# Kernel optimization log

Measured on AMD Instinct MI355X. Metric: run time of the kernel, lower is better.

The kernel has to match this reference:

```python
import math
import jax, jax.numpy as jnp
import numpy as np

EMBED = 512
HEADS = 8
EPS = 1e-5


def _ln(x, gamma, beta):
    mu = jnp.mean(x, axis=-1, keepdims=True)
    var = jnp.mean(jnp.square(x - mu), axis=-1, keepdims=True)
    return (x - mu) * jax.lax.rsqrt(var + EPS) * gamma + beta


def setup_inputs() -> dict:
    key = jax.random.key(0)
    ks = jax.random.split(key, 16)
    D = EMBED
    s = 0.02
    inp = {
        "moves_embeddings": jax.random.normal(ks[0], (4, 2048, D), dtype=jnp.float32),
        "wq": jax.random.normal(ks[1], (D, D), dtype=jnp.float32) * s,
        "bq": jnp.zeros((D,), jnp.float32),
        "wk": jax.random.normal(ks[2], (D, D), dtype=jnp.float32) * s,
        "bk": jnp.zeros((D,), jnp.float32),
        "wv": jax.random.normal(ks[3], (D, D), dtype=jnp.float32) * s,
        "bv": jnp.zeros((D,), jnp.float32),
        "wo": jax.random.normal(ks[4], (D, D), dtype=jnp.float32) * s,
        "bo": jnp.zeros((D,), jnp.float32),
        "w_up": jax.random.normal(ks[5], (D, 4 * D), dtype=jnp.float32) * s,
        "b_up": jnp.zeros((4 * D,), jnp.float32),
        "w_down": jax.random.normal(ks[6], (4 * D, D), dtype=jnp.float32) * s,
        "b_down": jnp.zeros((D,), jnp.float32),
        "g1": jnp.ones((D,), jnp.float32),
        "beta1": jnp.zeros((D,), jnp.float32),
        "g2": jnp.ones((D,), jnp.float32),
        "beta2": jnp.zeros((D,), jnp.float32),
    }
    return inp


def reference(moves_embeddings, wq, bq, wk, bk, wv, bv, wo, bo,
              w_up, b_up, w_down, b_down, g1, beta1, g2, beta2):
    x = moves_embeddings  # [B, S, D]
    B, S, D = x.shape
    Hd = D // HEADS
    # QKV projections, split heads -> [B, H, S, Hd]
    q = (x @ wq + bq).reshape(B, S, HEADS, Hd).transpose(0, 2, 1, 3)
    k = (x @ wk + bk).reshape(B, S, HEADS, Hd).transpose(0, 2, 1, 3)
    v = (x @ wv + bv).reshape(B, S, HEADS, Hd).transpose(0, 2, 1, 3)
    # NOTE: original scales by sqrt(embedding_dim), not sqrt(head_dim)
    scores = jnp.einsum('bhqd,bhkd->bhqk', q, k) / math.sqrt(D)
    attn = jax.nn.softmax(scores, axis=-1)
    ctx = jnp.einsum('bhqk,bhkd->bhqd', attn, v)
    ctx = ctx.transpose(0, 2, 1, 3).reshape(B, S, D)
    y = ctx @ wo + bo
    x = _ln(x + y, g1, beta1)
    # FFN with exact (erf) GELU, matching torch nn.GELU default
    h = jax.nn.gelu(x @ w_up + b_up, approximate=False)
    y = h @ w_down + b_down
    return _ln(x + y, g2, beta2)
```

## Files before the change

kernel.cpp:

```cpp
#include <hip/hip_runtime.h>
#include <math.h>

#define D 512
#define NHEADS 8
#define HD 64
#define SEQ 2048
#define BATCH 4
#define MROWS (BATCH*SEQ)
#define QKVSTR 1536
#define ATT_QSCALE 0.06376228841159383f

typedef short bf16x8 __attribute__((ext_vector_type(8)));
typedef float f32x4 __attribute__((ext_vector_type(4)));
typedef float f32x16 __attribute__((ext_vector_type(16)));

__device__ __forceinline__ ushort f2bf(float f) {
    union { float f; unsigned u; } v; v.f = f;
    unsigned r = (v.u + 0x7fffu + ((v.u >> 16) & 1u)) >> 16;
    return (ushort)r;
}
__device__ __forceinline__ float bf2f(ushort u) {
    union { unsigned u; float f; } v; v.u = ((unsigned)u) << 16; return v.f;
}

__device__ __forceinline__ unsigned cvt_pk_bf16(float lo, float hi_) {
    unsigned r;
    asm("v_cvt_pk_bf16_f32 %0, %1, %2" : "=v"(r) : "v"(lo), "v"(hi_));
    return r;
}

__device__ __forceinline__ float exp2_hw(float x) {
    float r;
    asm("v_exp_f32 %0, %1" : "=v"(r) : "v"(x));
    return r;
}

__device__ __forceinline__ void plswap(unsigned &a, unsigned &b) {
    asm("v_permlane32_swap_b32 %0, %1" : "+v"(a), "+v"(b));
}
__device__ __forceinline__ void plswapf(float &a, float &b) {
    union { float f; unsigned u; } ua, ub;
    ua.f = a; ub.f = b;
    asm("v_permlane32_swap_b32 %0, %1" : "+v"(ua.u), "+v"(ub.u));
    a = ua.f; b = ub.f;
}

__device__ __forceinline__ void gload16(const void* g, void* lds) {
    __builtin_amdgcn_global_load_lds(
        (const __attribute__((address_space(1))) unsigned int*)(uintptr_t)g,
        (__attribute__((address_space(3))) unsigned int*)(uintptr_t)lds,
        16, 0, 0);
}

__device__ __forceinline__ int xcd_swz(int wg, int nwg) {
    const int cpx = nwg >> 3;
    return (wg & 7) * cpx + (wg >> 3);
}

template<int GELU, int OBF16, int SPLITK>
__global__ __launch_bounds__(512)
void gemm_mfma8(const ushort* __restrict__ A, const ushort* __restrict__ Bt,
                const float* __restrict__ bias, void* __restrict__ Cp,
                void* __restrict__ Cp2, int M, int N, int K)
{
    __shared__ ushort As[2][128 * 64];
    __shared__ ushort Bs[2][128 * 64];

    const int tid = threadIdx.x;
    const int w = tid >> 6, lane = tid & 63;
    const int lr = lane & 15, lg = lane >> 4;
    const int wr = w >> 2, wc = w & 3;

    const int gx = gridDim.x;
    const int wg = xcd_swz(blockIdx.y * gx + blockIdx.x, gx * gridDim.y);
    const int row0 = (wg / gx) * 128, col0 = (wg % gx) * 128;

    const int kLen = SPLITK ? (K >> 1) : K;
    const int kOff = SPLITK ? blockIdx.z * kLen : 0;

    const int srow = lane >> 3;
    const int schunk = (lane & 7) ^ srow;

    const ushort* aSrc = A  + (size_t)(row0 + w * 16 + srow) * K + kOff + schunk * 8;
    const ushort* bSrc = Bt + (size_t)(col0 + w * 16 + srow) * K + kOff + schunk * 8;

    f32x4 acc[4][2] = {};

    auto STAGE = [&](int buf, int k0) {
        ushort* aD = &As[buf][(w * 16) * 64];
        ushort* bD = &Bs[buf][(w * 16) * 64];
        gload16(aSrc + k0,                 aD);
        gload16(aSrc + (size_t)8 * K + k0, aD + 8 * 64);
        gload16(bSrc + k0,                 bD);
        gload16(bSrc + (size_t)8 * K + k0, bD + 8 * 64);
    };

    auto COMPUTE = [&](int buf) {
        const ushort* AsB = As[buf];
        const ushort* BsB = Bs[buf];
        #pragma unroll
        for (int kc = 0; kc < 2; ++kc) {
            bf16x8 af[4], bfr[2];
            #pragma unroll
            for (int mt = 0; mt < 4; ++mt)
                af[mt] = *(const bf16x8*)&AsB[(wr * 64 + mt * 16 + lr) * 64 +
                                             (((kc * 4 + lg) ^ (lr & 7)) * 8)];
            #pragma unroll
            for (int nt = 0; nt < 2; ++nt)
                bfr[nt] = *(const bf16x8*)&BsB[(wc * 32 + nt * 16 + lr) * 64 +
                                              (((kc * 4 + lg) ^ (lr & 7)) * 8)];
            __builtin_amdgcn_s_setprio(1);
            #pragma unroll
            for (int mt = 0; mt < 4; ++mt)
                #pragma unroll
                for (int nt = 0; nt < 2; ++nt)
                    acc[mt][nt] = __builtin_amdgcn_mfma_f32_16x16x32_bf16(
                        af[mt], bfr[nt], acc[mt][nt], 0, 0, 0);
            __builtin_amdgcn_s_setprio(0);
        }
    };

    const int nk = kLen >> 6;
    STAGE(0, 0);
    __syncthreads();
    for (int t = 0; t < nk; ++t) {
        if (t + 1 < nk) STAGE((t + 1) & 1, (t + 1) << 6);
        COMPUTE(t & 1);
        __syncthreads();
    }

    float* Pp = SPLITK ? (blockIdx.z ? (float*)Cp2 : (float*)Cp) : (float*)Cp;
    #pragma unroll
    for (int nt = 0; nt < 2; ++nt) {
        const int col = col0 + wc * 32 + nt * 16 + lr;
        const float bv = SPLITK ? 0.f : bias[col];
        #pragma unroll
        for (int mt = 0; mt < 4; ++mt) {
            #pragma unroll
            for (int i = 0; i < 4; ++i) {
                float o = acc[mt][nt][i] + bv;
                if (GELU) o = 0.5f * o * (1.0f + erff(o * 0.70710678118654752f));
                const size_t idx = (size_t)(row0 + wr * 64 + mt * 16 + lg * 4 + i) * N + col;
                if (OBF16) ((ushort*)Cp)[idx] = f2bf(o);
                else       Pp[idx] = o;
            }
        }
    }
}

__global__ __launch_bounds__(512)
void gemm_qkv8(const ushort* __restrict__ A, const ushort* __restrict__ Bt,
               const float* __restrict__ bias, ushort* __restrict__ qkv,
               ushort* __restrict__ vt)
{
    __shared__ ushort As[2][128 * 64];
    __shared__ ushort Bs[2][128 * 64];

    const int tid = threadIdx.x;
    const int w = tid >> 6, lane = tid & 63;
    const int lr = lane & 15, lg = lane >> 4;
    const int wr = w >> 2, wc = w & 3;

    const int gx = gridDim.x;
    const int wg = xcd_swz(blockIdx.y * gx + blockIdx.x, gx * gridDim.y);
    const int row0 = (wg / gx) * 128, col0 = (wg % gx) * 128;

    const int K = 512;

    const int srow = lane >> 3;
    const int schunk = (lane & 7) ^ srow;

    const ushort* aSrc = A  + (size_t)(row0 + w * 16 + srow) * K + schunk * 8;
    const ushort* bSrc = Bt + (size_t)(col0 + w * 16 + srow) * K + schunk * 8;

    f32x4 acc[4][2] = {};

    auto STAGE = [&](int buf, int k0) {
        ushort* aD = &As[buf][(w * 16) * 64];
        ushort* bD = &Bs[buf][(w * 16) * 64];
        gload16(aSrc + k0,                 aD);
        gload16(aSrc + (size_t)8 * K + k0, aD + 8 * 64);
        gload16(bSrc + k0,                 bD);
        gload16(bSrc + (size_t)8 * K + k0, bD + 8 * 64);
    };

    auto COMPUTE = [&](int buf) {
        const ushort* AsB = As[buf];
        const ushort* BsB = Bs[buf];
        #pragma unroll
        for (int kc = 0; kc < 2; ++kc) {
            bf16x8 af[4], bfr[2];
            #pragma unroll
            for (int mt = 0; mt < 4; ++mt)
                af[mt] = *(const bf16x8*)&AsB[(wr * 64 + mt * 16 + lr) * 64 +
                                             (((kc * 4 + lg) ^ (lr & 7)) * 8)];
            #pragma unroll
            for (int nt = 0; nt < 2; ++nt)
                bfr[nt] = *(const bf16x8*)&BsB[(wc * 32 + nt * 16 + lr) * 64 +
                                              (((kc * 4 + lg) ^ (lr & 7)) * 8)];
            __builtin_amdgcn_s_setprio(1);
            #pragma unroll
            for (int mt = 0; mt < 4; ++mt)
                #pragma unroll
                for (int nt = 0; nt < 2; ++nt)
                    acc[mt][nt] = __builtin_amdgcn_mfma_f32_16x16x32_bf16(
                        af[mt], bfr[nt], acc[mt][nt], 0, 0, 0);
            __builtin_amdgcn_s_setprio(0);
        }
    };

    STAGE(0, 0);
    __syncthreads();
    for (int t = 0; t < 8; ++t) {
        if (t + 1 < 8) STAGE((t + 1) & 1, (t + 1) << 6);
        COMPUTE(t & 1);
        __syncthreads();
    }

    #pragma unroll
    for (int nt = 0; nt < 2; ++nt) {
        const int col = col0 + wc * 32 + nt * 16 + lr;
        const float bv = bias[col];
        if (col < 1024) {
            const float sc = (col < 512) ? ATT_QSCALE : 1.0f;
            #pragma unroll
            for (int mt = 0; mt < 4; ++mt) {
                #pragma unroll
                for (int i = 0; i < 4; ++i) {
                    const float o = (acc[mt][nt][i] + bv) * sc;
                    qkv[(size_t)(row0 + wr * 64 + mt * 16 + lg * 4 + i) * QKVSTR + col] = f2bf(o);
                }
            }
        } else {
            const int hh = (col - 1024) >> 6, d = (col - 1024) & 63;
            #pragma unroll
            for (int mt = 0; mt < 4; ++mt) {
                const int rowb = row0 + wr * 64 + mt * 16 + lg * 4;
                const int bb = rowb >> 11, ss = rowb & (SEQ - 1);
                ushort4 o4;
                o4.x = f2bf(acc[mt][nt][0] + bv);
                o4.y = f2bf(acc[mt][nt][1] + bv);
                o4.z = f2bf(acc[mt][nt][2] + bv);
                o4.w = f2bf(acc[mt][nt][3] + bv);
                *(ushort4*)&vt[((size_t)(bb * NHEADS + hh) * HD + d) * SEQ + ss] = o4;
            }
        }
    }
}

#define KBLK 64
#define NKT (1024 / KBLK)

__global__ __launch_bounds__(512, 4)
void attn_mfma(const ushort* __restrict__ qkv, const ushort* __restrict__ vt,
               ushort* __restrict__ ctx)
{
    __shared__ __align__(16) ushort smem[2][2][2][64 * 64];

    const int tid = threadIdx.x;
    const int lane = tid & 63;
    const int l32 = lane & 31, hi = lane >> 5;
    const int w = tid >> 6;
    const int qsub = w & 3, half = w >> 2;

    const int flat = blockIdx.x + 16 * (blockIdx.y + 8 * blockIdx.z);
    const int wg = xcd_swz(flat, 512);
    const int qt = wg & 15, h = (wg >> 4) & 7, b = wg >> 7;

    const int q0 = qt * 128 + qsub * 32;
    const int kbase = half * 1024;

    const size_t seqbase = (size_t)b * SEQ;
    const ushort* Qp = qkv + (seqbase + q0 + l32) * QKVSTR + h * HD;
    const ushort* Kg = qkv + seqbase * QKVSTR + 512 + h * HD;
    const ushort* Vg = vt + (size_t)(b * NHEADS + h) * HD * SEQ;

    bf16x8 qf[4];
    #pragma unroll
    for (int c = 0; c < 4; ++c) qf[c] = *(const bf16x8*)&Qp[c * 16 + hi * 8];

    const int srow = lane >> 3;
    const int sslot = (lane & 7) ^ srow;
    const ushort* pK = Kg + (size_t)(kbase + qsub * 16 + srow) * QKVSTR + sslot * 8;
    const ushort* pV = Vg + (size_t)(qsub * 16 + srow) * SEQ + kbase + sslot * 8;

    f32x16 o0 = {}, o1 = {};
    float l = 0.f;

    auto STAGE = [&](int buf) {
        ushort* dK = &smem[buf][half][0][(qsub * 16) * 64];
        ushort* dV = &smem[buf][half][1][(qsub * 16) * 64];
        gload16(pK,                      dK);
        gload16(pK + (size_t)8 * QKVSTR, dK + 8 * 64);
        gload16(pV,                      dV);
        gload16(pV + (size_t)8 * SEQ,    dV + 8 * 64);
        pK += (size_t)KBLK * QKVSTR;
        pV += KBLK;
    };

    auto COMPUTE = [&](int buf) {
        const ushort* KsH = &smem[buf][half][0][0];
        const ushort* VsH = &smem[buf][half][1][0];

        f32x16 s0 = {}, s1 = {};
        __builtin_amdgcn_s_setprio(1);
        #pragma unroll
        for (int c = 0; c < 4; ++c) {
            const bf16x8 kf0 = *(const bf16x8*)&KsH[l32 * 64 + (((2 * c + hi) ^ (l32 & 7)) * 8)];
            s0 = __builtin_amdgcn_mfma_f32_32x32x16_bf16(kf0, qf[c], s0, 0, 0, 0);
        }
        #pragma unroll
        for (int c = 0; c < 4; ++c) {
            const bf16x8 kf1 = *(const bf16x8*)&KsH[(32 + l32) * 64 + (((2 * c + hi) ^ (l32 & 7)) * 8)];
            s1 = __builtin_amdgcn_mfma_f32_32x32x16_bf16(kf1, qf[c], s1, 0, 0, 0);
        }
        __builtin_amdgcn_s_setprio(0);

        float ts = 0.f;
        #pragma unroll
        for (int r = 0; r < 16; ++r) {
            s0[r] = exp2_hw(s0[r]); ts += s0[r];
            s1[r] = exp2_hw(s1[r]); ts += s1[r];
        }
        l += ts;

        unsigned wp[16];
        #pragma unroll
        for (int j = 0; j < 8; ++j) wp[j]     = cvt_pk_bf16(s0[2 * j], s0[2 * j + 1]);
        #pragma unroll
        for (int j = 0; j < 8; ++j) wp[8 + j] = cvt_pk_bf16(s1[2 * j], s1[2 * j + 1]);
        plswap(wp[0], wp[2]);  plswap(wp[1], wp[3]);
        plswap(wp[4], wp[6]);  plswap(wp[5], wp[7]);
        plswap(wp[8], wp[10]); plswap(wp[9], wp[11]);
        plswap(wp[12], wp[14]); plswap(wp[13], wp[15]);
        union { unsigned u[4]; bf16x8 v; } pb[4];
        #pragma unroll
        for (int kg = 0; kg < 4; ++kg) {
            pb[kg].u[0] = wp[kg * 4 + 0];
            pb[kg].u[1] = wp[kg * 4 + 1];
            pb[kg].u[2] = wp[kg * 4 + 2];
            pb[kg].u[3] = wp[kg * 4 + 3];
        }

        __builtin_amdgcn_s_setprio(1);
        #pragma unroll
        for (int kg = 0; kg < 4; ++kg) {
            const bf16x8 vf0 = *(const bf16x8*)&VsH[l32 * 64 + (((2 * kg + hi) ^ (l32 & 7)) * 8)];
            o0 = __builtin_amdgcn_mfma_f32_32x32x16_bf16(vf0, pb[kg].v, o0, 0, 0, 0);
        }
        #pragma unroll
        for (int kg = 0; kg < 4; ++kg) {
            const bf16x8 vf1 = *(const bf16x8*)&VsH[(32 + l32) * 64 + (((2 * kg + hi) ^ (l32 & 7)) * 8)];
            o1 = __builtin_amdgcn_mfma_f32_32x32x16_bf16(vf1, pb[kg].v, o1, 0, 0, 0);
        }
        __builtin_amdgcn_s_setprio(0);
    };

    STAGE(0);
    __syncthreads();
    for (int tt = 0; tt < NKT; tt += 2) {
        if (tt + 1 < NKT) STAGE(1);
        COMPUTE(0);
        __syncthreads();
        if (tt + 2 < NKT) STAGE(0);
        COMPUTE(1);
        __syncthreads();
    }

    { float a_ = l, b_ = l; plswapf(a_, b_); l = a_ + b_; }

    float* so = (float*)smem;
    float* sl = (float*)((char*)smem + 4 * 64 * 33 * 4);
    if (half) {
        float* row = so + (qsub * 64 + lane) * 33;
        #pragma unroll
        for (int r = 0; r < 16; ++r) row[r] = o0[r];
        #pragma unroll
        for (int r = 0; r < 16; ++r) row[16 + r] = o1[r];
        sl[qsub * 64 + lane] = l;
    }
    __syncthreads();
    if (!half) {
        const float lb = sl[qsub * 64 + lane];
        const float* row = so + (qsub * 64 + lane) * 33;
        const float inv = 1.f / (l + lb);

        ushort* dst = ctx + (seqbase + q0 + l32) * D + h * HD;
        #pragma unroll
        for (int g = 0; g < 4; ++g) {
            ushort4 t0, t1;
            t0.x = f2bf((o0[g * 4 + 0] + row[g * 4 + 0]) * inv);
            t0.y = f2bf((o0[g * 4 + 1] + row[g * 4 + 1]) * inv);
            t0.z = f2bf((o0[g * 4 + 2] + row[g * 4 + 2]) * inv);
            t0.w = f2bf((o0[g * 4 + 3] + row[g * 4 + 3]) * inv);
            t1.x = f2bf((o1[g * 4 + 0] + row[16 + g * 4 + 0]) * inv);
            t1.y = f2bf((o1[g * 4 + 1] + row[16 + g * 4 + 1]) * inv);
            t1.z = f2bf((o1[g * 4 + 2] + row[16 + g * 4 + 2]) * inv);
            t1.w = f2bf((o1[g * 4 + 3] + row[16 + g * 4 + 3]) * inv);
            *(ushort4*)&dst[g * 8 + hi * 4]      = t0;
            *(ushort4*)&dst[32 + g * 8 + hi * 4] = t1;
        }
    }
}

template<int RESBF, int OUTBF>
__global__ __launch_bounds__(256)
void add_ln3(const void* __restrict__ res, const float* __restrict__ b0,
             const float* __restrict__ b1, const float* __restrict__ bias,
             const float* __restrict__ g, const float* __restrict__ beta,
             float* __restrict__ outf, ushort* __restrict__ outb)
{
    const int wave = threadIdx.x >> 6, lane = threadIdx.x & 63;
    const size_t row = (size_t)blockIdx.x * 4 + wave;

    float xr[8];
    if (RESBF) {
        const ushort* pr = (const ushort*)res + row * D + lane * 8;
        const ushort4 r0 = *(const ushort4*)pr;
        const ushort4 r1 = *(const ushort4*)(pr + 4);
        xr[0] = bf2f(r0.x); xr[1] = bf2f(r0.y); xr[2] = bf2f(r0.z); xr[3] = bf2f(r0.w);
        xr[4] = bf2f(r1.x); xr[5] = bf2f(r1.y); xr[6] = bf2f(r1.z); xr[7] = bf2f(r1.w);
    } else {
        const float* pr = (const float*)res + row * D + lane * 8;
        const float4 r0 = *(const float4*)pr;
        const float4 r1 = *(const float4*)(pr + 4);
        xr[0] = r0.x; xr[1] = r0.y; xr[2] = r0.z; xr[3] = r0.w;
        xr[4] = r1.x; xr[5] = r1.y; xr[6] = r1.z; xr[7] = r1.w;
    }

    const float* p0 = &b0[row * D + lane * 8];
    const float* p1 = &b1[row * D + lane * 8];
    const float4 c0 = *(const float4*)p0;
    const float4 c1 = *(const float4*)(p0 + 4);
    const float4 d0 = *(const float4*)p1;
    const float4 d1 = *(const float4*)(p1 + 4);
    const float4 bb0 = *(const float4*)&bias[lane * 8];
    const float4 bb1 = *(const float4*)&bias[lane * 8 + 4];

    float x[8];
    x[0] = xr[0] + c0.x + d0.x + bb0.x; x[1] = xr[1] + c0.y + d0.y + bb0.y;
    x[2] = xr[2] + c0.z + d0.z + bb0.z; x[3] = xr[3] + c0.w + d0.w + bb0.w;
    x[4] = xr[4] + c1.x + d1.x + bb1.x; x[5] = xr[5] + c1.y + d1.y + bb1.y;
    x[6] = xr[6] + c1.z + d1.z + bb1.z; x[7] = xr[7] + c1.w + d1.w + bb1.w;

    float sum = 0.f;
    #pragma unroll
    for (int i = 0; i < 8; ++i) sum += x[i];
    #pragma unroll
    for (int off = 32; off >= 1; off >>= 1) sum += __shfl_xor(sum, off);
    const float mu = sum * (1.0f / D);

    float vsum = 0.f;
    #pragma unroll
    for (int i = 0; i < 8; ++i) { const float dxe = x[i] - mu; vsum += dxe * dxe; }
    #pragma unroll
    for (int off = 32; off >= 1; off >>= 1) vsum += __shfl_xor(vsum, off);
    const float rs = rsqrtf(vsum * (1.0f / D) + 1e-5f);

    const float4 g0  = *(const float4*)&g[lane * 8];
    const float4 g1v = *(const float4*)&g[lane * 8 + 4];
    const float4 be0 = *(const float4*)&beta[lane * 8];
    const float4 be1 = *(const float4*)&beta[lane * 8 + 4];

    float o[8];
    o[0] = (x[0] - mu) * rs * g0.x  + be0.x;
    o[1] = (x[1] - mu) * rs * g0.y  + be0.y;
    o[2] = (x[2] - mu) * rs * g0.z  + be0.z;
    o[3] = (x[3] - mu) * rs * g0.w  + be0.w;
    o[4] = (x[4] - mu) * rs * g1v.x + be1.x;
    o[5] = (x[5] - mu) * rs * g1v.y + be1.y;
    o[6] = (x[6] - mu) * rs * g1v.z + be1.z;
    o[7] = (x[7] - mu) * rs * g1v.w + be1.w;

    if (OUTBF) {
        ushort4 lo, hi;
        lo.x = f2bf(o[0]); lo.y = f2bf(o[1]); lo.z = f2bf(o[2]); lo.w = f2bf(o[3]);
        hi.x = f2bf(o[4]); hi.y = f2bf(o[5]); hi.z = f2bf(o[6]); hi.w = f2bf(o[7]);
        ushort* pq = &outb[row * D + lane * 8];
        *(ushort4*)pq       = lo;
        *(ushort4*)(pq + 4) = hi;
    } else {
        float* po = &outf[row * D + lane * 8];
        *(float4*)po       = *(float4*)&o[0];
        *(float4*)(po + 4) = *(float4*)&o[4];
    }
}

__global__ __launch_bounds__(256)
void prep(const float* __restrict__ x, ushort* __restrict__ x_bf,
          const float* __restrict__ wq, const float* __restrict__ wk,
          const float* __restrict__ wv, const float* __restrict__ wo,
          const float* __restrict__ w_up, const float* __restrict__ w_down,
          ushort* __restrict__ Wt_qkv, ushort* __restrict__ Wt_o,
          ushort* __restrict__ Wt_up, ushort* __restrict__ Wt_down,
          const float* __restrict__ bq, const float* __restrict__ bk,
          const float* __restrict__ bv, float* __restrict__ b_qkv)
{
    const int bid = blockIdx.x;
    const int tid = threadIdx.x;

    if (bid < 2048) {
        const int i = bid * 256 + tid;
        const float4 a = *(const float4*)&x[(size_t)i * 8];
        const float4 b = *(const float4*)&x[(size_t)i * 8 + 4];
        ushort4 lo, hi;
        lo.x = f2bf(a.x); lo.y = f2bf(a.y); lo.z = f2bf(a.z); lo.w = f2bf(a.w);
        hi.x = f2bf(b.x); hi.y = f2bf(b.y); hi.z = f2bf(b.z); hi.w = f2bf(b.w);
        *(ushort4*)&x_bf[(size_t)i * 8]     = lo;
        *(ushort4*)&x_bf[(size_t)i * 8 + 4] = hi;
        return;
    }

    if (bid < 5120) {
        __shared__ float t[32][33];
        const int j = bid - 2048;
        const float* W; ushort* Wt; int N, stride, tI;
        if (j < 256)       { W = wq;     Wt = Wt_qkv;              N = 512;  stride = 512;  tI = j; }
        else if (j < 512)  { W = wk;     Wt = Wt_qkv + 512 * 512;  N = 512;  stride = 512;  tI = j - 256; }
        else if (j < 768)  { W = wv;     Wt = Wt_qkv + 1024 * 512; N = 512;  stride = 512;  tI = j - 512; }
        else if (j < 1024) { W = wo;     Wt = Wt_o;                N = 512;  stride = 512;  tI = j - 768; }
        else if (j < 2048) { W = w_up;   Wt = Wt_up;               N = 2048; stride = 512;  tI = j - 1024; }
        else               { W = w_down; Wt = Wt_down;             N = 512;  stride = 2048; tI = j - 2048; }
        const int ntn = N >> 5;
        const int n0 = (tI % ntn) * 32, k0 = (tI / ntn) * 32;
        const int r = tid >> 5, c = tid & 31;
        #pragma unroll
        for (int i = 0; i < 4; ++i)
            t[r + i * 8][c] = W[(size_t)(k0 + r + i * 8) * N + n0 + c];
        __syncthreads();
        #pragma unroll
        for (int i = 0; i < 4; ++i)
            Wt[(size_t)(n0 + r + i * 8) * stride + k0 + c] = f2bf(t[c][r + i * 8]);
        return;
    }

    const int i = (bid - 5120) * 256 + tid;
    if (i < 1536)
        b_qkv[i] = (i < 512) ? bq[i] : (i < 1024 ? bk[i - 512] : bv[i - 1024]);
}

extern "C" void kernel_launch(void* const* d_in, const int* in_sizes, int n_in,
                              void* d_out, int out_size, void* d_ws, size_t ws_size,
                              hipStream_t stream)
{
    const float* x      = (const float*)d_in[0];
    const float* wq     = (const float*)d_in[1];
    const float* bq     = (const float*)d_in[2];
    const float* wk     = (const float*)d_in[3];
    const float* bk     = (const float*)d_in[4];
    const float* wv     = (const float*)d_in[5];
    const float* bv     = (const float*)d_in[6];
    const float* wo     = (const float*)d_in[7];
    const float* bo     = (const float*)d_in[8];
    const float* w_up   = (const float*)d_in[9];
    const float* b_up   = (const float*)d_in[10];
    const float* w_down = (const float*)d_in[11];
    const float* b_down = (const float*)d_in[12];
    const float* g1     = (const float*)d_in[13];
    const float* beta1  = (const float*)d_in[14];
    const float* g2     = (const float*)d_in[15];
    const float* beta2  = (const float*)d_in[16];
    float* out = (float*)d_out;

    char* wsb = (char*)d_ws;
    #define WS(ofs_mb) (wsb + ((size_t)(ofs_mb) << 20))
    ushort* Wt_qkv  = (ushort*)WS(0);
    ushort* Wt_o    = (ushort*)WS(2);
    ushort* Wt_up   = (ushort*)WS(3);
    ushort* Wt_down = (ushort*)WS(5);
    float*  b_qkv   = (float*) WS(7);
    ushort* x_bf    = (ushort*)WS(8);
    ushort* qkv_bf  = (ushort*)WS(16);
    ushort* vt_bf   = (ushort*)WS(40);
    ushort* ctx_bf  = (ushort*)WS(48);
    float*  yp0     = (float*) WS(8);
    float*  yp1     = (float*) WS(24);
    ushort* x1_bf   = (ushort*)WS(40);
    ushort* h_bf    = (ushort*)WS(8);
    float*  y2p0    = (float*) WS(64);
    float*  y2p1    = (float*) WS(80);
    #undef WS

    const dim3 blk(256), blk8(512);

    prep<<<dim3(5126), blk, 0, stream>>>(x, x_bf, wq, wk, wv, wo, w_up, w_down,
                                         Wt_qkv, Wt_o, Wt_up, Wt_down,
                                         bq, bk, bv, b_qkv);

    gemm_qkv8<<<dim3(12, 64), blk8, 0, stream>>>(x_bf, Wt_qkv, b_qkv, qkv_bf, vt_bf);

    attn_mfma<<<dim3(SEQ / 128, NHEADS, BATCH), blk8, 0, stream>>>(qkv_bf, vt_bf, ctx_bf);

    gemm_mfma8<0, 0, 1><<<dim3(4, 64, 2), blk8, 0, stream>>>(ctx_bf, Wt_o, nullptr, yp0, yp1, MROWS, 512, 512);
    add_ln3<0, 1><<<dim3(MROWS / 4), blk, 0, stream>>>(x, yp0, yp1, bo, g1, beta1, nullptr, x1_bf);

    gemm_mfma8<1, 1, 0><<<dim3(16, 64), blk8, 0, stream>>>(x1_bf, Wt_up, b_up, h_bf, nullptr, MROWS, 2048, 512);
    gemm_mfma8<0, 0, 1><<<dim3(4, 64, 2), blk8, 0, stream>>>(h_bf, Wt_down, nullptr, y2p0, y2p1, MROWS, 512, 2048);
    add_ln3<1, 0><<<dim3(MROWS / 4), blk, 0, stream>>>(x1_bf, y2p0, y2p1, b_down, g2, beta2, out, nullptr);
}
```

Measured before the change: 150.1 us.

## Interleave attention softmax halves with PV MFMAs and use fast polynomial GELU

The attention inner step is split into two halves: exp, bf16 packing and lane swaps for the first 32 keys are followed by their PV MFMAs before the second half's exp work. This lets the compiler overlap transcendental ALU work with matrix ops and narrows the setprio window. Separately, the FFN-up GELU epilogue replaces erff with the Abramowitz-Stegun polynomial erf approximation, using hardware rcp and exp2. That makes the epilogue cheaper at the cost of about 1e-7 absolute erf error, which is negligible given the bf16 output.

```diff
diff --git a/kernel.cpp b/kernel.cpp
--- a/kernel.cpp
+++ b/kernel.cpp
@@ -34,6 +34,24 @@
     asm("v_exp_f32 %0, %1" : "=v"(r) : "v"(x));
     return r;
 }
+__device__ __forceinline__ float rcp_hw(float x) {
+    float r;
+    asm("v_rcp_f32 %0, %1" : "=v"(r) : "v"(x));
+    return r;
+}
+
+__device__ __forceinline__ float gelu_fast(float x) {
+    const float z = fabsf(x) * 0.70710678118654752f;
+    const float t = rcp_hw(fmaf(0.3275911f, z, 1.0f));
+    float p = fmaf(1.061405429f, t, -1.453152027f);
+    p = fmaf(p, t, 1.421413741f);
+    p = fmaf(p, t, -0.284496736f);
+    p = fmaf(p, t, 0.254829592f);
+    const float e = exp2_hw(-z * z * 1.4426950408889634f);
+    const float erfz = 1.0f - p * t * e;
+    const float s = copysignf(erfz, x);
+    return 0.5f * x * (1.0f + s);
+}
 
 __device__ __forceinline__ void plswap(unsigned &a, unsigned &b) {
     asm("v_permlane32_swap_b32 %0, %1" : "+v"(a), "+v"(b));
@@ -139,7 +157,7 @@
             #pragma unroll
             for (int i = 0; i < 4; ++i) {
                 float o = acc[mt][nt][i] + bv;
-                if (GELU) o = 0.5f * o * (1.0f + erff(o * 0.70710678118654752f));
+                if (GELU) o = gelu_fast(o);
                 const size_t idx = (size_t)(row0 + wr * 64 + mt * 16 + lg * 4 + i) * N + col;
                 if (OBF16) ((ushort*)Cp)[idx] = f2bf(o);
                 else       Pp[idx] = o;
@@ -303,57 +321,60 @@
         const ushort* VsH = &smem[buf][half][1][0];
 
         f32x16 s0 = {}, s1 = {};
+
         __builtin_amdgcn_s_setprio(1);
         #pragma unroll
         for (int c = 0; c < 4; ++c) {
             const bf16x8 kf0 = *(const bf16x8*)&KsH[l32 * 64 + (((2 * c + hi) ^ (l32 & 7)) * 8)];
             s0 = __builtin_amdgcn_mfma_f32_32x32x16_bf16(kf0, qf[c], s0, 0, 0, 0);
         }
+        __builtin_amdgcn_s_setprio(0);
+
         #pragma unroll
         for (int c = 0; c < 4; ++c) {
             const bf16x8 kf1 = *(const bf16x8*)&KsH[(32 + l32) * 64 + (((2 * c + hi) ^ (l32 & 7)) * 8)];
             s1 = __builtin_amdgcn_mfma_f32_32x32x16_bf16(kf1, qf[c], s1, 0, 0, 0);
         }
-        __builtin_amdgcn_s_setprio(0);
 
         float ts = 0.f;
-        #pragma unroll
-        for (int r = 0; r < 16; ++r) {
-            s0[r] = exp2_hw(s0[r]); ts += s0[r];
-            s1[r] = exp2_hw(s1[r]); ts += s1[r];
-        }
-        l += ts;
-
         unsigned wp[16];
-        #pragma unroll
-        for (int j = 0; j < 8; ++j) wp[j]     = cvt_pk_bf16(s0[2 * j], s0[2 * j + 1]);
-        #pragma unroll
-        for (int j = 0; j < 8; ++j) wp[8 + j] = cvt_pk_bf16(s1[2 * j], s1[2 * j + 1]);
+        union { unsigned u[4]; bf16x8 v; } pb[4];
+
+        #pragma unroll
+        for (int r = 0; r < 16; ++r) { s0[r] = exp2_hw(s0[r]); ts += s0[r]; }
+        #pragma unroll
+        for (int j = 0; j < 8; ++j) wp[j] = cvt_pk_bf16(s0[2 * j], s0[2 * j + 1]);
         plswap(wp[0], wp[2]);  plswap(wp[1], wp[3]);
         plswap(wp[4], wp[6]);  plswap(wp[5], wp[7]);
-        plswap(wp[8], wp[10]); plswap(wp[9], wp[11]);
-        plswap(wp[12], wp[14]); plswap(wp[13], wp[15]);
-        union { unsigned u[4]; bf16x8 v; } pb[4];
-        #pragma unroll
-        for (int kg = 0; kg < 4; ++kg) {
-            pb[kg].u[0] = wp[kg * 4 + 0];
-            pb[kg].u[1] = wp[kg * 4 + 1];
-            pb[kg].u[2] = wp[kg * 4 + 2];
-            pb[kg].u[3] = wp[kg * 4 + 3];
-        }
-
-        __builtin_amdgcn_s_setprio(1);
-        #pragma unroll
-        for (int kg = 0; kg < 4; ++kg) {
+        pb[0].u[0] = wp[0]; pb[0].u[1] = wp[1]; pb[0].u[2] = wp[2]; pb[0].u[3] = wp[3];
+        pb[1].u[0] = wp[4]; pb[1].u[1] = wp[5]; pb[1].u[2] = wp[6]; pb[1].u[3] = wp[7];
+
+        #pragma unroll
+        for (int kg = 0; kg < 2; ++kg) {
             const bf16x8 vf0 = *(const bf16x8*)&VsH[l32 * 64 + (((2 * kg + hi) ^ (l32 & 7)) * 8)];
             o0 = __builtin_amdgcn_mfma_f32_32x32x16_bf16(vf0, pb[kg].v, o0, 0, 0, 0);
-        }
-        #pragma unroll
-        for (int kg = 0; kg < 4; ++kg) {
             const bf16x8 vf1 = *(const bf16x8*)&VsH[(32 + l32) * 64 + (((2 * kg + hi) ^ (l32 & 7)) * 8)];
             o1 = __builtin_amdgcn_mfma_f32_32x32x16_bf16(vf1, pb[kg].v, o1, 0, 0, 0);
         }
-        __builtin_amdgcn_s_setprio(0);
+
+        #pragma unroll
+        for (int r = 0; r < 16; ++r) { s1[r] = exp2_hw(s1[r]); ts += s1[r]; }
+        #pragma unroll
+        for (int j = 0; j < 8; ++j) wp[8 + j] = cvt_pk_bf16(s1[2 * j], s1[2 * j + 1]);
+        plswap(wp[8], wp[10]);  plswap(wp[9], wp[11]);
+        plswap(wp[12], wp[14]); plswap(wp[13], wp[15]);
+        pb[2].u[0] = wp[8];  pb[2].u[1] = wp[9];  pb[2].u[2] = wp[10]; pb[2].u[3] = wp[11];
+        pb[3].u[0] = wp[12]; pb[3].u[1] = wp[13]; pb[3].u[2] = wp[14]; pb[3].u[3] = wp[15];
+
+        #pragma unroll
+        for (int kg = 2; kg < 4; ++kg) {
+            const bf16x8 vf0 = *(const bf16x8*)&VsH[l32 * 64 + (((2 * kg + hi) ^ (l32 & 7)) * 8)];
+            o0 = __builtin_amdgcn_mfma_f32_32x32x16_bf16(vf0, pb[kg].v, o0, 0, 0, 0);
+            const bf16x8 vf1 = *(const bf16x8*)&VsH[(32 + l32) * 64 + (((2 * kg + hi) ^ (l32 & 7)) * 8)];
+            o1 = __builtin_amdgcn_mfma_f32_32x32x16_bf16(vf1, pb[kg].v, o1, 0, 0, 0);
+        }
+
+        l += ts;
     };
 
     STAGE(0);
```

New measurement: 148.2 us. Within noise of the previous version (-1.3%).
